# Optimization experiments

Hardware: AMD Instinct MI355X
Metric: run time of the kernel (lower is better)

The kernel has to match this reference:

```python
import jax, jax.numpy as jnp
import numpy as np

D_MODEL = 1024
EXPAND = 2
D_INNER = D_MODEL * EXPAND
KERNEL = 4
EPS = 1e-5


def setup_inputs() -> dict:
    key = jax.random.key(0)
    ks = jax.random.split(key, 8)
    B, L = 2, 4096
    x = jax.random.normal(ks[0], (B, L, D_MODEL), dtype=jnp.float32)
    norm_w = jnp.ones((D_MODEL,), jnp.float32)
    norm_b = jnp.zeros((D_MODEL,), jnp.float32)
    # torch Linear weight layout [out, in]
    in_proj_w = jax.random.normal(ks[1], (2 * D_INNER, D_MODEL), jnp.float32) / np.sqrt(D_MODEL)
    # depthwise Conv1d weight [d_inner, 1, K]
    conv_w = jax.random.normal(ks[2], (D_INNER, 1, KERNEL), jnp.float32) / np.sqrt(KERNEL)
    conv_b = jax.random.normal(ks[3], (D_INNER,), jnp.float32) * 0.02
    gate_w = jax.random.normal(ks[4], (D_INNER, D_INNER), jnp.float32) / np.sqrt(D_INNER)
    gate_b = jnp.zeros((D_INNER,), jnp.float32)
    out_proj_w = jax.random.normal(ks[5], (D_MODEL, D_INNER), jnp.float32) / np.sqrt(D_INNER)
    return {"x": x, "norm_w": norm_w, "norm_b": norm_b, "in_proj_w": in_proj_w,
            "conv_w": conv_w, "conv_b": conv_b, "gate_w": gate_w, "gate_b": gate_b,
            "out_proj_w": out_proj_w}


def _layernorm(x, w, b):
    mu = jnp.mean(x, axis=-1, keepdims=True)
    var = jnp.var(x, axis=-1, keepdims=True)
    return (x - mu) * jax.lax.rsqrt(var + EPS) * w + b


def _glru(x, norm_w, norm_b, in_proj_w, conv_w, conv_b, gate_w, gate_b, out_proj_w):
    B, L, D = x.shape
    residual = x
    xn = _layernorm(x, norm_w, norm_b)
    xz = jnp.einsum('bld,ed->ble', xn, in_proj_w)  # [B,L,2*d_inner]
    x_inner, z = jnp.split(xz, 2, axis=-1)
    # causal depthwise conv: torch pads 3 both sides then slices [:L] == left-pad 3
    lhs = jnp.transpose(x_inner, (0, 2, 1))  # [B, C, L]
    conv = jax.lax.conv_general_dilated(
        lhs, conv_w, window_strides=(1,), padding=[(KERNEL - 1, 0)],
        feature_group_count=D_INNER,
        dimension_numbers=('NCH', 'OIH', 'NCH'))
    x_conv = jnp.transpose(conv, (0, 2, 1)) + conv_b  # [B, L, C]
    x_conv = jax.nn.silu(x_conv)
    a = jax.nn.sigmoid(jnp.einsum('blc,ec->ble', x_conv, gate_w) + gate_b)
    b = (1.0 - a) * x_conv
    # h_t = a_t * h_{t-1} + b_t, h_0 prior = 0 -> parallel associative scan
    def combine(e1, e2):
        a1, b1 = e1
        a2, b2 = e2
        return a1 * a2, a2 * b1 + b2
    _, y = jax.lax.associative_scan(combine, (a, b), axis=1)
    y = y * jax.nn.silu(z)
    return residual + jnp.einsum('blc,dc->bld', y, out_proj_w)


def reference(x, norm_w, norm_b, in_proj_w, conv_w, conv_b, gate_w, gate_b, out_proj_w):
    return _glru(x, norm_w, norm_b, in_proj_w, conv_w, conv_b, gate_w, gate_b, out_proj_w)
```

## Files before the change

kernel.cpp:

```cpp
#include <hip/hip_runtime.h>
#include <cstdint>

#define D_MODEL 1024
#define D_INNER 2048
#define LSEQ    4096
#define BATCH   2
#define M_ROWS  (BATCH * LSEQ)
#define CHUNK   128
#define NCHUNK  (LSEQ / CHUNK)

typedef unsigned short u16;
typedef __bf16 bf16x8 __attribute__((ext_vector_type(8)));
typedef float f32x4 __attribute__((ext_vector_type(4)));
typedef u16 u16x4 __attribute__((ext_vector_type(4)));

__device__ __forceinline__ u16 f2bf(float f) {
  union { float f; unsigned u; } x; x.f = f;
  unsigned u = x.u;
  unsigned r = (u + 0x7FFFu + ((u >> 16) & 1u)) >> 16;
  return (u16)r;
}
__device__ __forceinline__ float bf2f(u16 h) {
  union { unsigned u; float f; } x; x.u = ((unsigned)h) << 16;
  return x.f;
}
__device__ __forceinline__ float sigmoidf_(float v) { return 1.0f / (1.0f + expf(-v)); }
__device__ __forceinline__ float siluf_(float v)    { return v / (1.0f + expf(-v)); }

__device__ __forceinline__ void gl_lds16(const void* g, void* l) {
  __builtin_amdgcn_global_load_lds(
      (const __attribute__((address_space(1))) void*)g,
      (__attribute__((address_space(3))) void*)l, 16, 0, 0);
}

#define SBAR()   asm volatile("s_barrier" ::: "memory")
#define WAITV0() asm volatile("s_waitcnt vmcnt(0)" ::: "memory")
#define WAITV6() asm volatile("s_waitcnt vmcnt(6)" ::: "memory")

__global__ void __launch_bounds__(256)
cast_bf16_kernel(const float* __restrict__ in, u16* __restrict__ out, int n4) {
  int i = blockIdx.x * 256 + threadIdx.x;
  if (i < n4) {
    float4 v = ((const float4*)in)[i];
    u16x4 o;
    o.x = f2bf(v.x); o.y = f2bf(v.y); o.z = f2bf(v.z); o.w = f2bf(v.w);
    ((u16x4*)out)[i] = o;
  }
}

__global__ void __launch_bounds__(256)
ln_kernel(const float* __restrict__ x, const float* __restrict__ w,
          const float* __restrict__ b, u16* __restrict__ xn) {
  const int row = blockIdx.x;
  const int t = threadIdx.x;
  const float4 v = ((const float4*)(x + (size_t)row * D_MODEL))[t];
  float s  = v.x + v.y + v.z + v.w;
  float ss = v.x * v.x + v.y * v.y + v.z * v.z + v.w * v.w;
#pragma unroll
  for (int o = 32; o > 0; o >>= 1) {
    s  += __shfl_xor(s, o);
    ss += __shfl_xor(ss, o);
  }
  __shared__ float red[8];
  const int wid = t >> 6, lane = t & 63;
  if (lane == 0) { red[wid] = s; red[4 + wid] = ss; }
  __syncthreads();
  s  = red[0] + red[1] + red[2] + red[3];
  ss = red[4] + red[5] + red[6] + red[7];
  const float mu  = s * (1.0f / D_MODEL);
  const float var = ss * (1.0f / D_MODEL) - mu * mu;
  const float rs  = rsqrtf(var + 1e-5f);
  const float4 wv = ((const float4*)w)[t];
  const float4 bv = ((const float4*)b)[t];
  u16x4 o4;
  o4.x = f2bf((v.x - mu) * rs * wv.x + bv.x);
  o4.y = f2bf((v.y - mu) * rs * wv.y + bv.y);
  o4.z = f2bf((v.z - mu) * rs * wv.z + bv.z);
  o4.w = f2bf((v.w - mu) * rs * wv.w + bv.w);
  ((u16x4*)(xn + (size_t)row * D_MODEL))[t] = o4;
}

#define MFMA_BF16 __builtin_amdgcn_mfma_f32_16x16x32_bf16

template<int EPI>
__global__ void __launch_bounds__(512)
gemm256(const u16* __restrict__ A, const u16* __restrict__ Bm,
        int M, int N, int K,
        const float* __restrict__ ef, float* __restrict__ of,
        u16* __restrict__ ob0, u16* __restrict__ ob1) {
  __shared__ __align__(1024) char lds[131072];
  const int tid  = threadIdx.x;
  const int wid  = tid >> 6, lane = tid & 63;
  const int nbx  = N >> 8;
  const int nwg  = nbx * (M >> 8);
  const int bid  = blockIdx.x;
  const int cpx  = nwg >> 3;
  const int swz  = (bid & 7) * cpx + (bid >> 3);
  const int bx   = swz % nbx, by = swz / nbx;
  const size_t m0 = (size_t)by << 8, n0 = (size_t)bx << 8;

  const int wr = wid >> 2, wc = wid & 3;
  const size_t rb = (size_t)K * 2;
  const size_t rj = (size_t)64 * rb;

  const int srow  = lane >> 3;
  const int sslot = ((lane & 7) ^ srow) << 4;
  const char* gA = (const char*)A  + (m0 + (size_t)(wid * 8 + srow)) * rb + sslot;
  const char* gB = (const char*)Bm + (n0 + (size_t)(wid * 8 + srow)) * rb + sslot;
  const int sdst = wid * 1024;

  const int q    = lane >> 4;
  const int r15  = lane & 15;
  const int cswz0 = (q * 16)      ^ ((lane & 7) << 4);
  const int cswz1 = (64 + q * 16) ^ ((lane & 7) << 4);
  const int paoff = (wr * 128 + r15) * 128;
  const int pboff = (wc * 64  + r15) * 128;

  f32x4 acc[8][4] = {};
  bf16x8 afL[4][2], afH[4][2], b0r[2][2], b1r[2][2];
  const int nk = K >> 6;

  {
    const char* a = gA; const char* b = gB;
#pragma unroll
    for (int i = 0; i < 4; ++i) {
      gl_lds16(a, lds + sdst + i * 8192);
      gl_lds16(b, lds + 65536 + sdst + i * 8192);
      a += rj; b += rj;
    }
  }
  WAITV0();
  SBAR();
  {
    const char* At = lds;
    const char* Bt = lds + 65536;
#pragma unroll
    for (int mi = 0; mi < 4; ++mi) {
      afL[mi][0] = *(const bf16x8*)(At + paoff + mi * 2048 + cswz0);
      afL[mi][1] = *(const bf16x8*)(At + paoff + mi * 2048 + cswz1);
    }
#pragma unroll
    for (int ni = 0; ni < 2; ++ni) {
      b0r[ni][0] = *(const bf16x8*)(Bt + pboff + ni * 2048 + cswz0);
      b0r[ni][1] = *(const bf16x8*)(Bt + pboff + ni * 2048 + cswz1);
    }
  }

  size_t kb = 128;
  for (int t = 0; t < nk; ++t) {
    const int cur = t & 1;
    const char* At = lds + cur * 32768;
    const char* Bt = lds + 65536 + cur * 32768;
    char* An = lds + (cur ^ 1) * 32768;
    char* Bn = lds + 65536 + (cur ^ 1) * 32768;
    const bool pf = (t + 1 < nk);

    if (pf) {
      gl_lds16(gA + kb,          An + sdst);
      gl_lds16(gA + kb + 2 * rj, An + sdst + 16384);
      gl_lds16(gB + kb,          Bn + sdst);
      gl_lds16(gB + kb + rj,     Bn + sdst + 8192);
      gl_lds16(gB + kb + 2 * rj, Bn + sdst + 16384);
      gl_lds16(gB + kb + 3 * rj, Bn + sdst + 24576);
    }
#pragma unroll
    for (int ni = 0; ni < 2; ++ni) {
      b1r[ni][0] = *(const bf16x8*)(Bt + pboff + (ni + 2) * 2048 + cswz0);
      b1r[ni][1] = *(const bf16x8*)(Bt + pboff + (ni + 2) * 2048 + cswz1);
    }
    __builtin_amdgcn_s_setprio(1);
#pragma unroll
    for (int mi = 0; mi < 4; ++mi)
#pragma unroll
      for (int ni = 0; ni < 2; ++ni) {
        acc[mi][ni] = MFMA_BF16(afL[mi][0], b0r[ni][0], acc[mi][ni], 0, 0, 0);
        acc[mi][ni] = MFMA_BF16(afL[mi][1], b0r[ni][1], acc[mi][ni], 0, 0, 0);
      }
    __builtin_amdgcn_s_setprio(0);
    if (pf) { WAITV6(); } else { WAITV0(); }
    SBAR();

#pragma unroll
    for (int mi = 0; mi < 4; ++mi) {
      afH[mi][0] = *(const bf16x8*)(At + paoff + (mi + 4) * 2048 + cswz0);
      afH[mi][1] = *(const bf16x8*)(At + paoff + (mi + 4) * 2048 + cswz1);
    }
    __builtin_amdgcn_s_setprio(1);
#pragma unroll
    for (int mi = 0; mi < 4; ++mi)
#pragma unroll
      for (int ni = 0; ni < 2; ++ni) {
        acc[mi][ni + 2] = MFMA_BF16(afL[mi][0], b1r[ni][0], acc[mi][ni + 2], 0, 0, 0);
        acc[mi][ni + 2] = MFMA_BF16(afL[mi][1], b1r[ni][1], acc[mi][ni + 2], 0, 0, 0);
      }
    __builtin_amdgcn_s_setprio(0);
    SBAR();

    __builtin_amdgcn_s_setprio(1);
#pragma unroll
    for (int mi = 0; mi < 4; ++mi)
#pragma unroll
      for (int ni = 0; ni < 2; ++ni) {
        acc[mi + 4][ni] = MFMA_BF16(afH[mi][0], b0r[ni][0], acc[mi + 4][ni], 0, 0, 0);
        acc[mi + 4][ni] = MFMA_BF16(afH[mi][1], b0r[ni][1], acc[mi + 4][ni], 0, 0, 0);
      }
    __builtin_amdgcn_s_setprio(0);
    WAITV0();
    SBAR();

    if (pf) {
      gl_lds16(gA + kb + rj,     An + sdst + 8192);
      gl_lds16(gA + kb + 3 * rj, An + sdst + 24576);
#pragma unroll
      for (int mi = 0; mi < 4; ++mi) {
        afL[mi][0] = *(const bf16x8*)(An + paoff + mi * 2048 + cswz0);
        afL[mi][1] = *(const bf16x8*)(An + paoff + mi * 2048 + cswz1);
      }
#pragma unroll
      for (int ni = 0; ni < 2; ++ni) {
        b0r[ni][0] = *(const bf16x8*)(Bn + pboff + ni * 2048 + cswz0);
        b0r[ni][1] = *(const bf16x8*)(Bn + pboff + ni * 2048 + cswz1);
      }
    }
    __builtin_amdgcn_s_setprio(1);
#pragma unroll
    for (int mi = 0; mi < 4; ++mi)
#pragma unroll
      for (int ni = 0; ni < 2; ++ni) {
        acc[mi + 4][ni + 2] = MFMA_BF16(afH[mi][0], b1r[ni][0], acc[mi + 4][ni + 2], 0, 0, 0);
        acc[mi + 4][ni + 2] = MFMA_BF16(afH[mi][1], b1r[ni][1], acc[mi + 4][ni + 2], 0, 0, 0);
      }
    __builtin_amdgcn_s_setprio(0);
    SBAR();
    kb += 128;
  }

  const int c0 = lane & 15;
  const int r0 = (lane >> 4) << 2;
  const bool isz = (EPI == 0) && (n0 >= (size_t)D_INNER);
#pragma unroll
  for (int mi = 0; mi < 8; ++mi) {
#pragma unroll
    for (int ni = 0; ni < 4; ++ni) {
#pragma unroll
      for (int rg = 0; rg < 4; ++rg) {
        const size_t row = m0 + (size_t)(wr * 128 + mi * 16 + r0 + rg);
        const size_t col = n0 + (size_t)(wc * 64 + ni * 16 + c0);
        const float v = acc[mi][ni][rg];
        if (EPI == 0) {
          if (!isz) ob0[row * D_INNER + col] = f2bf(v);
          else      ob1[row * D_INNER + (col - D_INNER)] = f2bf(siluf_(v));
        } else if (EPI == 1) {
          ob0[row * (size_t)N + col] = f2bf(v);
        } else {
          of[row * (size_t)N + col] = v + ef[row * (size_t)N + col];
        }
      }
    }
  }
}

__global__ void __launch_bounds__(256)
conv_silu_kernel(const u16* __restrict__ xin, const float* __restrict__ cw,
                 const float* __restrict__ cb, u16* __restrict__ xc) {
  const int c   = blockIdx.x * 256 + threadIdx.x;
  const int l0  = blockIdx.y * 8;
  const int bat = blockIdx.z;
  const size_t base = ((size_t)bat * LSEQ) * D_INNER + c;
  const float w0 = cw[c * 4 + 0], w1 = cw[c * 4 + 1], w2 = cw[c * 4 + 2], w3 = cw[c * 4 + 3];
  const float bb = cb[c];
  float v[11];
#pragma unroll
  for (int i = 0; i < 11; ++i) {
    const int l = l0 - 3 + i;
    v[i] = (l >= 0) ? bf2f(xin[base + (size_t)l * D_INNER]) : 0.0f;
  }
#pragma unroll
  for (int r = 0; r < 8; ++r) {
    const float acc = bb + w0 * v[r] + w1 * v[r + 1] + w2 * v[r + 2] + w3 * v[r + 3];
    xc[base + (size_t)(l0 + r) * D_INNER] = f2bf(siluf_(acc));
  }
}

__global__ void __launch_bounds__(256)
scan_a_kernel(const u16* __restrict__ g, const u16* __restrict__ xc,
              const float* __restrict__ gbias,
              float* __restrict__ cA, float* __restrict__ cB) {
  const int c   = (blockIdx.x * 256 + threadIdx.x) * 2;
  const int ch  = blockIdx.y;
  const int bat = blockIdx.z;
  const float bb0 = gbias[c], bb1 = gbias[c + 1];
  size_t idx = ((size_t)bat * LSEQ + (size_t)ch * CHUNK) * D_INNER + c;
  float pA0 = 1.0f, hB0 = 0.0f, pA1 = 1.0f, hB1 = 0.0f;
  for (int t = 0; t < CHUNK; ++t) {
    const ushort2 gg = *(const ushort2*)(g + idx);
    const ushort2 xx = *(const ushort2*)(xc + idx);
    const float a0 = sigmoidf_(bf2f(gg.x) + bb0);
    const float a1 = sigmoidf_(bf2f(gg.y) + bb1);
    pA0 *= a0; hB0 = a0 * hB0 + (1.0f - a0) * bf2f(xx.x);
    pA1 *= a1; hB1 = a1 * hB1 + (1.0f - a1) * bf2f(xx.y);
    idx += D_INNER;
  }
  const size_t o = ((size_t)bat * NCHUNK + ch) * D_INNER + c;
  *(float2*)(cA + o) = make_float2(pA0, pA1);
  *(float2*)(cB + o) = make_float2(hB0, hB1);
}

__global__ void __launch_bounds__(256)
scan_b_kernel(const float* __restrict__ cA, const float* __restrict__ cB,
              float* __restrict__ carry) {
  const int tid = blockIdx.x * 256 + threadIdx.x;
  const int bat = tid >> 11;
  const int c   = tid & (D_INNER - 1);
  float h = 0.0f;
  const size_t base = (size_t)bat * NCHUNK * D_INNER + c;
  for (int i = 0; i < NCHUNK; ++i) {
    const size_t o = base + (size_t)i * D_INNER;
    carry[o] = h;
    h = cA[o] * h + cB[o];
  }
}

__global__ void __launch_bounds__(256)
scan_c_kernel(const u16* __restrict__ g, const u16* __restrict__ xc,
              const u16* __restrict__ sz, const float* __restrict__ gbias,
              const float* __restrict__ carry, u16* __restrict__ yg) {
  const int c   = (blockIdx.x * 256 + threadIdx.x) * 2;
  const int ch  = blockIdx.y;
  const int bat = blockIdx.z;
  const float bb0 = gbias[c], bb1 = gbias[c + 1];
  const float2 h2 = *(const float2*)(carry + ((size_t)bat * NCHUNK + ch) * D_INNER + c);
  float h0 = h2.x, h1 = h2.y;
  size_t idx = ((size_t)bat * LSEQ + (size_t)ch * CHUNK) * D_INNER + c;
  for (int t = 0; t < CHUNK; ++t) {
    const ushort2 gg = *(const ushort2*)(g + idx);
    const ushort2 xx = *(const ushort2*)(xc + idx);
    const ushort2 zz = *(const ushort2*)(sz + idx);
    const float a0 = sigmoidf_(bf2f(gg.x) + bb0);
    const float a1 = sigmoidf_(bf2f(gg.y) + bb1);
    h0 = a0 * h0 + (1.0f - a0) * bf2f(xx.x);
    h1 = a1 * h1 + (1.0f - a1) * bf2f(xx.y);
    ushort2 o2;
    o2.x = f2bf(h0 * bf2f(zz.x));
    o2.y = f2bf(h1 * bf2f(zz.y));
    *(ushort2*)(yg + idx) = o2;
    idx += D_INNER;
  }
}

extern "C" void kernel_launch(void* const* d_in, const int* in_sizes, int n_in,
                              void* d_out, int out_size, void* d_ws, size_t ws_size,
                              hipStream_t stream) {
  const float* x         = (const float*)d_in[0];
  const float* norm_w    = (const float*)d_in[1];
  const float* norm_b    = (const float*)d_in[2];
  const float* in_proj_w = (const float*)d_in[3];
  const float* conv_w    = (const float*)d_in[4];
  const float* conv_b    = (const float*)d_in[5];
  const float* gate_w    = (const float*)d_in[6];
  const float* gate_b    = (const float*)d_in[7];
  const float* out_proj_w= (const float*)d_in[8];
  float* out = (float*)d_out;

  char* p = (char*)d_ws;
  u16* xn      = (u16*)p; p += (size_t)M_ROWS * D_MODEL * 2;
  u16* w_in    = (u16*)p; p += (size_t)2 * D_INNER * D_MODEL * 2;
  u16* w_gate  = (u16*)p; p += (size_t)D_INNER * D_INNER * 2;
  u16* w_out   = (u16*)p; p += (size_t)D_MODEL * D_INNER * 2;
  u16* x_inner = (u16*)p; p += (size_t)M_ROWS * D_INNER * 2;
  u16* szb     = (u16*)p; p += (size_t)M_ROWS * D_INNER * 2;
  u16* xconv   = (u16*)p; p += (size_t)M_ROWS * D_INNER * 2;
  u16* gbuf    = (u16*)p; p += (size_t)M_ROWS * D_INNER * 2;
  u16* yg      = (u16*)p; p += (size_t)M_ROWS * D_INNER * 2;
  float* cA    = (float*)p; p += (size_t)BATCH * NCHUNK * D_INNER * 4;
  float* cB    = (float*)p; p += (size_t)BATCH * NCHUNK * D_INNER * 4;
  float* carry = (float*)p; p += (size_t)BATCH * NCHUNK * D_INNER * 4;
  if ((size_t)(p - (char*)d_ws) > ws_size) return;

  cast_bf16_kernel<<<dim3(2 * D_INNER * D_MODEL / 4 / 256), 256, 0, stream>>>(in_proj_w, w_in, 2 * D_INNER * D_MODEL / 4);
  cast_bf16_kernel<<<dim3(D_INNER * D_INNER / 4 / 256), 256, 0, stream>>>(gate_w, w_gate, D_INNER * D_INNER / 4);
  cast_bf16_kernel<<<dim3(D_MODEL * D_INNER / 4 / 256), 256, 0, stream>>>(out_proj_w, w_out, D_MODEL * D_INNER / 4);

  ln_kernel<<<dim3(M_ROWS), 256, 0, stream>>>(x, norm_w, norm_b, xn);

  gemm256<0><<<dim3((M_ROWS / 256) * (2 * D_INNER / 256)), 512, 0, stream>>>(
      xn, w_in, M_ROWS, 2 * D_INNER, D_MODEL, nullptr, nullptr, x_inner, szb);

  conv_silu_kernel<<<dim3(D_INNER / 256, LSEQ / 8, BATCH), 256, 0, stream>>>(x_inner, conv_w, conv_b, xconv);

  gemm256<1><<<dim3((M_ROWS / 256) * (D_INNER / 256)), 512, 0, stream>>>(
      xconv, w_gate, M_ROWS, D_INNER, D_INNER, nullptr, nullptr, gbuf, nullptr);

  scan_a_kernel<<<dim3(D_INNER / 512, NCHUNK, BATCH), 256, 0, stream>>>(gbuf, xconv, gate_b, cA, cB);
  scan_b_kernel<<<dim3(BATCH * D_INNER / 256), 256, 0, stream>>>(cA, cB, carry);
  scan_c_kernel<<<dim3(D_INNER / 512, NCHUNK, BATCH), 256, 0, stream>>>(gbuf, xconv, szb, gate_b, carry, yg);

  gemm256<2><<<dim3((M_ROWS / 256) * (D_MODEL / 256)), 512, 0, stream>>>(
      yg, w_out, M_ROWS, D_MODEL, D_INNER, x, out, nullptr, nullptr);
}
```

Measured before the change: 348.8 us.

## Restructure GEMM LDS layout into k-half sub-tiles and use 256x128 tiles for out_proj

```diff
diff --git a/kernel.cpp b/kernel.cpp
--- a/kernel.cpp
+++ b/kernel.cpp
@@ -35,7 +35,6 @@
 
 #define SBAR()   asm volatile("s_barrier" ::: "memory")
 #define WAITV0() asm volatile("s_waitcnt vmcnt(0)" ::: "memory")
-#define WAITV6() asm volatile("s_waitcnt vmcnt(6)" ::: "memory")
 
 __global__ void __launch_bounds__(256)
 cast_bf16_kernel(const float* __restrict__ in, u16* __restrict__ out, int n4) {
@@ -82,156 +81,137 @@
 
 #define MFMA_BF16 __builtin_amdgcn_mfma_f32_16x16x32_bf16
 
-template<int EPI>
+template<int EPI, int BN>
 __global__ void __launch_bounds__(512)
-gemm256(const u16* __restrict__ A, const u16* __restrict__ Bm,
-        int M, int N, int K,
-        const float* __restrict__ ef, float* __restrict__ of,
-        u16* __restrict__ ob0, u16* __restrict__ ob1) {
-  __shared__ __align__(1024) char lds[131072];
+gemmK(const u16* __restrict__ A, const u16* __restrict__ Bm,
+      int M, int N, int K,
+      const float* __restrict__ ef, float* __restrict__ of,
+      u16* __restrict__ ob0, u16* __restrict__ ob1) {
+  constexpr int NI    = BN / 64;
+  constexpr int LB    = BN / 128;
+  constexpr int BHALF = BN * 64;
+  constexpr int BUFS  = 32768 + 2 * BHALF;
+  __shared__ __align__(1024) char lds[2 * BUFS];
   const int tid  = threadIdx.x;
   const int wid  = tid >> 6, lane = tid & 63;
-  const int nbx  = N >> 8;
+  const int nbx  = N / BN;
   const int nwg  = nbx * (M >> 8);
   const int bid  = blockIdx.x;
   const int cpx  = nwg >> 3;
   const int swz  = (bid & 7) * cpx + (bid >> 3);
   const int bx   = swz % nbx, by = swz / nbx;
-  const size_t m0 = (size_t)by << 8, n0 = (size_t)bx << 8;
+  const size_t m0 = (size_t)by << 8;
+  const size_t n0 = (size_t)bx * BN;
 
   const int wr = wid >> 2, wc = wid & 3;
-  const size_t rb = (size_t)K * 2;
-  const size_t rj = (size_t)64 * rb;
-
-  const int srow  = lane >> 3;
-  const int sslot = ((lane & 7) ^ srow) << 4;
-  const char* gA = (const char*)A  + (m0 + (size_t)(wid * 8 + srow)) * rb + sslot;
-  const char* gB = (const char*)Bm + (n0 + (size_t)(wid * 8 + srow)) * rb + sslot;
-  const int sdst = wid * 1024;
-
-  const int q    = lane >> 4;
-  const int r15  = lane & 15;
-  const int cswz0 = (q * 16)      ^ ((lane & 7) << 4);
-  const int cswz1 = (64 + q * 16) ^ ((lane & 7) << 4);
-  const int paoff = (wr * 128 + r15) * 128;
-  const int pboff = (wc * 64  + r15) * 128;
-
-  f32x4 acc[8][4] = {};
-  bf16x8 afL[4][2], afH[4][2], b0r[2][2], b1r[2][2];
+  const size_t rb  = (size_t)K * 2;
+  const size_t rj16 = 16 * rb;
+
+  const char* gAs = (const char*)A  + (m0 + (size_t)(wid * 32 + (lane >> 2))) * rb + ((lane & 3) << 4);
+  const char* gBs = (const char*)Bm + (n0 + (size_t)(wid * 16 * LB + (lane >> 2))) * rb + ((lane & 3) << 4);
+  const int sA = wid * 2048;
+  const int sB = wid * (LB * 1024);
+
+  const int q = lane >> 4, r15 = lane & 15;
+  const int aoff = (wr * 128 + r15) * 64 + q * 16;
+  const int boff = (wc * (BN / 4) + r15) * 64 + q * 16;
+
+  f32x4 acc[8][NI] = {};
   const int nk = K >> 6;
 
-  {
-    const char* a = gA; const char* b = gB;
-#pragma unroll
-    for (int i = 0; i < 4; ++i) {
-      gl_lds16(a, lds + sdst + i * 8192);
-      gl_lds16(b, lds + 65536 + sdst + i * 8192);
-      a += rj; b += rj;
-    }
+#pragma unroll
+  for (int kkh = 0; kkh < 2; ++kkh) {
+#pragma unroll
+    for (int j = 0; j < 2; ++j)
+      gl_lds16(gAs + kkh * 64 + j * rj16, lds + kkh * 16384 + sA + j * 1024);
+#pragma unroll
+    for (int j = 0; j < LB; ++j)
+      gl_lds16(gBs + kkh * 64 + j * rj16, lds + 32768 + kkh * BHALF + sB + j * 1024);
   }
   WAITV0();
   SBAR();
-  {
-    const char* At = lds;
-    const char* Bt = lds + 65536;
-#pragma unroll
-    for (int mi = 0; mi < 4; ++mi) {
-      afL[mi][0] = *(const bf16x8*)(At + paoff + mi * 2048 + cswz0);
-      afL[mi][1] = *(const bf16x8*)(At + paoff + mi * 2048 + cswz1);
-    }
-#pragma unroll
-    for (int ni = 0; ni < 2; ++ni) {
-      b0r[ni][0] = *(const bf16x8*)(Bt + pboff + ni * 2048 + cswz0);
-      b0r[ni][1] = *(const bf16x8*)(Bt + pboff + ni * 2048 + cswz1);
-    }
-  }
 
   size_t kb = 128;
   for (int t = 0; t < nk; ++t) {
     const int cur = t & 1;
-    const char* At = lds + cur * 32768;
-    const char* Bt = lds + 65536 + cur * 32768;
-    char* An = lds + (cur ^ 1) * 32768;
-    char* Bn = lds + 65536 + (cur ^ 1) * 32768;
+    const char* cb = lds + cur * BUFS;
+    char* nbb = lds + (cur ^ 1) * BUFS;
     const bool pf = (t + 1 < nk);
-
-    if (pf) {
-      gl_lds16(gA + kb,          An + sdst);
-      gl_lds16(gA + kb + 2 * rj, An + sdst + 16384);
-      gl_lds16(gB + kb,          Bn + sdst);
-      gl_lds16(gB + kb + rj,     Bn + sdst + 8192);
-      gl_lds16(gB + kb + 2 * rj, Bn + sdst + 16384);
-      gl_lds16(gB + kb + 3 * rj, Bn + sdst + 24576);
-    }
-#pragma unroll
-    for (int ni = 0; ni < 2; ++ni) {
-      b1r[ni][0] = *(const bf16x8*)(Bt + pboff + (ni + 2) * 2048 + cswz0);
-      b1r[ni][1] = *(const bf16x8*)(Bt + pboff + (ni + 2) * 2048 + cswz1);
-    }
+    bf16x8 af[4], bf0[NI], bf1[NI];
+
+    if (pf) {
+      gl_lds16(gAs + kb,        nbb + sA);
+      gl_lds16(gAs + kb + rj16, nbb + sA + 1024);
+    }
+#pragma unroll
+    for (int mi = 0; mi < 4; ++mi) af[mi] = *(const bf16x8*)(cb + aoff + mi * 1024);
+#pragma unroll
+    for (int ni = 0; ni < NI; ++ni) bf0[ni] = *(const bf16x8*)(cb + 32768 + boff + ni * 1024);
     __builtin_amdgcn_s_setprio(1);
 #pragma unroll
     for (int mi = 0; mi < 4; ++mi)
 #pragma unroll
-      for (int ni = 0; ni < 2; ++ni) {
-        acc[mi][ni] = MFMA_BF16(afL[mi][0], b0r[ni][0], acc[mi][ni], 0, 0, 0);
-        acc[mi][ni] = MFMA_BF16(afL[mi][1], b0r[ni][1], acc[mi][ni], 0, 0, 0);
-      }
+      for (int ni = 0; ni < NI; ++ni)
+        acc[mi][ni] = MFMA_BF16(af[mi], bf0[ni], acc[mi][ni], 0, 0, 0);
     __builtin_amdgcn_s_setprio(0);
-    if (pf) { WAITV6(); } else { WAITV0(); }
+
+    if (pf) {
+#pragma unroll
+      for (int j = 0; j < LB; ++j)
+        gl_lds16(gBs + kb + j * rj16, nbb + 32768 + sB + j * 1024);
+    }
+#pragma unroll
+    for (int mi = 0; mi < 4; ++mi) af[mi] = *(const bf16x8*)(cb + 4096 + aoff + mi * 1024);
+    if (pf) {
+      if constexpr (LB == 2) asm volatile("s_waitcnt vmcnt(4)" ::: "memory");
+      else                   asm volatile("s_waitcnt vmcnt(3)" ::: "memory");
+    } else {
+      WAITV0();
+    }
     SBAR();
-
-#pragma unroll
-    for (int mi = 0; mi < 4; ++mi) {
-      afH[mi][0] = *(const bf16x8*)(At + paoff + (mi + 4) * 2048 + cswz0);
-      afH[mi][1] = *(const bf16x8*)(At + paoff + (mi + 4) * 2048 + cswz1);
-    }
     __builtin_amdgcn_s_setprio(1);
 #pragma unroll
     for (int mi = 0; mi < 4; ++mi)
 #pragma unroll
-      for (int ni = 0; ni < 2; ++ni) {
-        acc[mi][ni + 2] = MFMA_BF16(afL[mi][0], b1r[ni][0], acc[mi][ni + 2], 0, 0, 0);
-        acc[mi][ni + 2] = MFMA_BF16(afL[mi][1], b1r[ni][1], acc[mi][ni + 2], 0, 0, 0);
-      }
+      for (int ni = 0; ni < NI; ++ni)
+        acc[4 + mi][ni] = MFMA_BF16(af[mi], bf0[ni], acc[4 + mi][ni], 0, 0, 0);
     __builtin_amdgcn_s_setprio(0);
+
+    if (pf) {
+      gl_lds16(gAs + kb + 64,        nbb + 16384 + sA);
+      gl_lds16(gAs + kb + 64 + rj16, nbb + 16384 + sA + 1024);
+    }
+#pragma unroll
+    for (int mi = 0; mi < 4; ++mi) af[mi] = *(const bf16x8*)(cb + 16384 + aoff + mi * 1024);
+#pragma unroll
+    for (int ni = 0; ni < NI; ++ni) bf1[ni] = *(const bf16x8*)(cb + 32768 + BHALF + boff + ni * 1024);
+    __builtin_amdgcn_s_setprio(1);
+#pragma unroll
+    for (int mi = 0; mi < 4; ++mi)
+#pragma unroll
+      for (int ni = 0; ni < NI; ++ni)
+        acc[mi][ni] = MFMA_BF16(af[mi], bf1[ni], acc[mi][ni], 0, 0, 0);
+    __builtin_amdgcn_s_setprio(0);
+
+    if (pf) {
+#pragma unroll
+      for (int j = 0; j < LB; ++j)
+        gl_lds16(gBs + kb + 64 + j * rj16, nbb + 32768 + BHALF + sB + j * 1024);
+    }
+#pragma unroll
+    for (int mi = 0; mi < 4; ++mi) af[mi] = *(const bf16x8*)(cb + 16384 + 4096 + aoff + mi * 1024);
+    if (pf) {
+      if constexpr (LB == 2) asm volatile("s_waitcnt vmcnt(4)" ::: "memory");
+      else                   asm volatile("s_waitcnt vmcnt(3)" ::: "memory");
+    }
     SBAR();
-
     __builtin_amdgcn_s_setprio(1);
 #pragma unroll
     for (int mi = 0; mi < 4; ++mi)
 #pragma unroll
-      for (int ni = 0; ni < 2; ++ni) {
-        acc[mi + 4][ni] = MFMA_BF16(afH[mi][0], b0r[ni][0], acc[mi + 4][ni], 0, 0, 0);
-        acc[mi + 4][ni] = MFMA_BF16(afH[mi][1], b0r[ni][1], acc[mi + 4][ni], 0, 0, 0);
-      }
+      for (int ni = 0; ni < NI; ++ni)
+        acc[4 + mi][ni] = MFMA_BF16(af[mi], bf1[ni], acc[4 + mi][ni], 0, 0, 0);
     __builtin_amdgcn_s_setprio(0);
-    WAITV0();
-    SBAR();
-
-    if (pf) {
-      gl_lds16(gA + kb + rj,     An + sdst + 8192);
-      gl_lds16(gA + kb + 3 * rj, An + sdst + 24576);
-#pragma unroll
-      for (int mi = 0; mi < 4; ++mi) {
-        afL[mi][0] = *(const bf16x8*)(An + paoff + mi * 2048 + cswz0);
-        afL[mi][1] = *(const bf16x8*)(An + paoff + mi * 2048 + cswz1);
-      }
-#pragma unroll
-      for (int ni = 0; ni < 2; ++ni) {
-        b0r[ni][0] = *(const bf16x8*)(Bn + pboff + ni * 2048 + cswz0);
-        b0r[ni][1] = *(const bf16x8*)(Bn + pboff + ni * 2048 + cswz1);
-      }
-    }
-    __builtin_amdgcn_s_setprio(1);
-#pragma unroll
-    for (int mi = 0; mi < 4; ++mi)
-#pragma unroll
-      for (int ni = 0; ni < 2; ++ni) {
-        acc[mi + 4][ni + 2] = MFMA_BF16(afH[mi][0], b1r[ni][0], acc[mi + 4][ni + 2], 0, 0, 0);
-        acc[mi + 4][ni + 2] = MFMA_BF16(afH[mi][1], b1r[ni][1], acc[mi + 4][ni + 2], 0, 0, 0);
-      }
-    __builtin_amdgcn_s_setprio(0);
-    SBAR();
     kb += 128;
   }
 
@@ -239,14 +219,14 @@
   const int r0 = (lane >> 4) << 2;
   const bool isz = (EPI == 0) && (n0 >= (size_t)D_INNER);
 #pragma unroll
-  for (int mi = 0; mi < 8; ++mi) {
-#pragma unroll
-    for (int ni = 0; ni < 4; ++ni) {
+  for (int ai = 0; ai < 8; ++ai) {
+#pragma unroll
+    for (int ni = 0; ni < NI; ++ni) {
 #pragma unroll
       for (int rg = 0; rg < 4; ++rg) {
-        const size_t row = m0 + (size_t)(wr * 128 + mi * 16 + r0 + rg);
-        const size_t col = n0 + (size_t)(wc * 64 + ni * 16 + c0);
-        const float v = acc[mi][ni][rg];
+        const size_t row = m0 + (size_t)(wr * 128 + ai * 16 + r0 + rg);
+        const size_t col = n0 + (size_t)(wc * (BN / 4) + ni * 16 + c0);
+        const float v = acc[ai][ni][rg];
         if (EPI == 0) {
           if (!isz) ob0[row * D_INNER + col] = f2bf(v);
           else      ob1[row * D_INNER + (col - D_INNER)] = f2bf(siluf_(v));
@@ -383,18 +363,18 @@
 
   ln_kernel<<<dim3(M_ROWS), 256, 0, stream>>>(x, norm_w, norm_b, xn);
 
-  gemm256<0><<<dim3((M_ROWS / 256) * (2 * D_INNER / 256)), 512, 0, stream>>>(
+  gemmK<0, 256><<<dim3((M_ROWS / 256) * (2 * D_INNER / 256)), 512, 0, stream>>>(
       xn, w_in, M_ROWS, 2 * D_INNER, D_MODEL, nullptr, nullptr, x_inner, szb);
 
   conv_silu_kernel<<<dim3(D_INNER / 256, LSEQ / 8, BATCH), 256, 0, stream>>>(x_inner, conv_w, conv_b, xconv);
 
-  gemm256<1><<<dim3((M_ROWS / 256) * (D_INNER / 256)), 512, 0, stream>>>(
+  gemmK<1, 256><<<dim3((M_ROWS / 256) * (D_INNER / 256)), 512, 0, stream>>>(
       xconv, w_gate, M_ROWS, D_INNER, D_INNER, nullptr, nullptr, gbuf, nullptr);
 
   scan_a_kernel<<<dim3(D_INNER / 512, NCHUNK, BATCH), 256, 0, stream>>>(gbuf, xconv, gate_b, cA, cB);
   scan_b_kernel<<<dim3(BATCH * D_INNER / 256), 256, 0, stream>>>(cA, cB, carry);
   scan_c_kernel<<<dim3(D_INNER / 512, NCHUNK, BATCH), 256, 0, stream>>>(gbuf, xconv, szb, gate_b, carry, yg);
 
-  gemm256<2><<<dim3((M_ROWS / 256) * (D_MODEL / 256)), 512, 0, stream>>>(
+  gemmK<2, 128><<<dim3((M_ROWS / 256) * (D_MODEL / 128)), 512, 0, stream>>>(
       yg, w_out, M_ROWS, D_MODEL, D_INNER, x, out, nullptr, nullptr);
 }
```

Result: no change. 343.1 us (-1.7%).
